# Kernel optimization log

Hardware: AMD Instinct MI355X
Metric: run time of the kernel (lower is better)

Reference implementation:

```python
import jax, jax.numpy as jnp
import numpy as np

N, M, K = 100000, 50000, 8   # num vertices, num hyperedges, fixed hyperedge size
DIN, DOUT = 128, 128

def setup_inputs() -> dict:
    key = jax.random.key(0)
    k1, k2, k3 = jax.random.split(key, 3)
    X = jax.random.normal(k1, (N, DIN), jnp.float32)
    vertex = jax.random.randint(k2, (M * K,), 0, N)          # member vertices, flattened
    edges = jnp.repeat(jnp.arange(M), K)                     # hyperedge id per entry (sorted)
    W = jax.random.normal(k3, (DIN, DOUT), jnp.float32) / np.sqrt(DIN)
    b = jnp.zeros((DOUT,), jnp.float32)
    return {"X": X, "vertex": vertex, "edges": edges, "W": W, "b": b}

def reference(X, vertex, edges, W, b):
    # theta: Linear(in, out) applied BEFORE graph construction (as in dhg.HyperGCNConv)
    Y = X @ W + b                              # [N, DOUT]
    verts = vertex.reshape(M, K)               # hyperedge membership (edges = repeat(arange(M), K))
    feats = Y[verts]                           # [M, K, DOUT] gather
    # pairwise squared distances within each hyperedge
    sq = jnp.sum(feats * feats, axis=-1)                      # [M, K]
    d2 = sq[:, :, None] + sq[:, None, :] - 2.0 * jnp.einsum('mkd,mld->mkl', feats, feats)
    flat = jnp.argmax(d2.reshape(M, K * K), axis=1)
    ui, vi = flat // K, flat % K                              # argmax-distance pair positions
    u = jnp.take_along_axis(verts, ui[:, None], 1)[:, 0]      # [M]
    v = jnp.take_along_axis(verts, vi[:, None], 1)[:, 0]      # [M]
    w = jnp.float32(1.0 / (2 * K - 3))                        # HyperGCN mediator weight
    pos = jnp.arange(K)
    med = ((pos[None, :] != ui[:, None]) & (pos[None, :] != vi[:, None])).astype(Y.dtype)  # [M,K]
    # graph edges: (u,v) + (u,m),(v,m) for each mediator m; masked entries get weight 0
    src = jnp.concatenate([u, jnp.repeat(u, K), jnp.repeat(v, K)])
    dst = jnp.concatenate([v, verts.reshape(-1), verts.reshape(-1)])
    wts = jnp.concatenate([jnp.full((M,), w, Y.dtype), (med * w).reshape(-1), (med * w).reshape(-1)])
    # GCN smoothing: D^{-1/2} (A + I) D^{-1/2} Y with symmetric A, duplicate edges summed
    deg = jnp.ones((N,), Y.dtype).at[src].add(wts).at[dst].add(wts)
    dinv = jax.lax.rsqrt(deg)
    Xs = Y * dinv[:, None]
    out = Xs                                                  # self-loop term
    out = out.at[dst].add(wts[:, None] * Xs[src])
    out = out.at[src].add(wts[:, None] * Xs[dst])
    out = out * dinv[:, None]
    return jax.nn.relu(out)                                   # is_last=False -> ReLU (dropout=0)
```

## Files before the change

kernel.cpp:

```cpp
#include <hip/hip_runtime.h>
#include <hip/hip_bf16.h>

#define NV 100000
#define ME 50000
#define NINC (ME * 8)
#define NBLK ((NV + 255) / 256)
constexpr float WMED = 1.0f / 13.0f;

typedef __attribute__((ext_vector_type(8))) short bf16x8;
typedef __attribute__((ext_vector_type(4))) float f32x4;

static __device__ inline void cvt_split8(const float4& a, const float4& b,
                                         bf16x8& hi, bf16x8& lo) {
    const float v[8] = {a.x, a.y, a.z, a.w, b.x, b.y, b.z, b.w};
    #pragma unroll
    for (int j = 0; j < 8; ++j) {
        __hip_bfloat16 h = __float2bfloat16(v[j]);
        const float hf = __bfloat162float(h);
        __hip_bfloat16 l = __float2bfloat16(v[j] - hf);
        union { __hip_bfloat16 b; short s; } uh{h}, ul{l};
        hi[j] = uh.s;
        lo[j] = ul.s;
    }
}

__global__ __launch_bounds__(256) void k_wsplit(const float* __restrict__ W,
                                                short* __restrict__ Wg) {
    const int idx = blockIdx.x * 256 + threadIdx.x;
    const int k = idx >> 7;
    const int c = idx & 127;
    const float w = W[idx];
    __hip_bfloat16 h = __float2bfloat16(w);
    const float hf = __bfloat162float(h);
    __hip_bfloat16 l = __float2bfloat16(w - hf);
    const int cb = c >> 6, gp = (c >> 4) & 3, m = c & 15;
    const int s = k >> 5, qq = (k >> 3) & 3, j = k & 7;
    const int base = cb * 1024 + (s * 4 + gp) * 64 + qq * 16 + m;
    union { __hip_bfloat16 b; short s; } uh{h}, ul{l};
    Wg[(long)base * 8 + j] = uh.s;
    Wg[(long)(2048 + base) * 8 + j] = ul.s;
}

__global__ __launch_bounds__(512, 4) void k_gemm(const float* __restrict__ X,
                                                 const uint4* __restrict__ Wg,
                                                 const float* __restrict__ bias,
                                                 float* __restrict__ Y,
                                                 __hip_bfloat16* __restrict__ Ybf) {
    __shared__ uint4 sW[2048];
    const int t = threadIdx.x;
    const int wv = t >> 6;
    const int L  = t & 63;
    const int m  = L & 15;
    const int q  = L >> 4;

    const int rb = blockIdx.x >> 1;
    const int cb = blockIdx.x & 1;

    #pragma unroll
    for (int f = 0; f < 4; ++f) {
        const int fi = f * 512 + t;
        const int mat = fi >> 10, loc = fi & 1023;
        sW[fi] = Wg[(long)mat * 2048 + cb * 1024 + loc];
    }

    const int row_base = rb * 256 + wv * 32;
    int r0 = row_base + m;      if (r0 > NV - 1) r0 = NV - 1;
    int r1 = row_base + 16 + m; if (r1 > NV - 1) r1 = NV - 1;
    const float* p0 = X + (long)r0 * 128 + q * 8;
    const float* p1 = X + (long)r1 * 128 + q * 8;

    float4 A[4][4];
    #pragma unroll
    for (int s = 0; s < 4; ++s) {
        A[s][0] = *(const float4*)(p0 + s * 32);
        A[s][1] = *(const float4*)(p0 + s * 32 + 4);
        A[s][2] = *(const float4*)(p1 + s * 32);
        A[s][3] = *(const float4*)(p1 + s * 32 + 4);
    }
    __syncthreads();

    const bf16x8* sWf = (const bf16x8*)sW;

    f32x4 acc[2][4];
    #pragma unroll
    for (int tt = 0; tt < 2; ++tt)
        #pragma unroll
        for (int g = 0; g < 4; ++g)
            acc[tt][g] = (f32x4){0.f, 0.f, 0.f, 0.f};

    #pragma unroll
    for (int s = 0; s < 4; ++s) {
        bf16x8 ah0, al0, ah1, al1;
        cvt_split8(A[s][0], A[s][1], ah0, al0);
        cvt_split8(A[s][2], A[s][3], ah1, al1);
        #pragma unroll
        for (int g = 0; g < 4; ++g) {
            const bf16x8 bh = sWf[(s * 4 + g) * 64 + L];
            const bf16x8 bl = sWf[1024 + (s * 4 + g) * 64 + L];
            acc[0][g] = __builtin_amdgcn_mfma_f32_16x16x32_bf16(ah0, bh, acc[0][g], 0, 0, 0);
            acc[0][g] = __builtin_amdgcn_mfma_f32_16x16x32_bf16(ah0, bl, acc[0][g], 0, 0, 0);
            acc[0][g] = __builtin_amdgcn_mfma_f32_16x16x32_bf16(al0, bh, acc[0][g], 0, 0, 0);
            acc[1][g] = __builtin_amdgcn_mfma_f32_16x16x32_bf16(ah1, bh, acc[1][g], 0, 0, 0);
            acc[1][g] = __builtin_amdgcn_mfma_f32_16x16x32_bf16(ah1, bl, acc[1][g], 0, 0, 0);
            acc[1][g] = __builtin_amdgcn_mfma_f32_16x16x32_bf16(al1, bh, acc[1][g], 0, 0, 0);
        }
    }

    #pragma unroll
    for (int g = 0; g < 4; ++g) {
        const int col = cb * 64 + g * 16 + m;
        const float bc = bias[col];
        #pragma unroll
        for (int tt = 0; tt < 2; ++tt) {
            #pragma unroll
            for (int r = 0; r < 4; ++r) {
                const int row = row_base + tt * 16 + q * 4 + r;
                const float v = acc[tt][g][r] + bc;
                const float vn = __shfl_xor(v, 1);
                if (row < NV) {
                    Y[(long)row * 128 + col] = v;
                    if ((L & 1) == 0) {
                        __hip_bfloat162 h2;
                        h2.x = __float2bfloat16(v);
                        h2.y = __float2bfloat16(vn);
                        *(__hip_bfloat162*)(Ybf + (long)row * 128 + col) = h2;
                    }
                }
            }
        }
    }
}

__global__ __launch_bounds__(256) void k_edge(const float* __restrict__ Y,
                                              const int* __restrict__ vertex,
                                              int* __restrict__ uvpos) {
    __shared__ float sF[4][8 * 132];
    const int wid = threadIdx.x >> 6;
    const int lane = threadIdx.x & 63;
    const int m = blockIdx.x * 4 + wid;
    float* F = sF[wid];

    int verts[8];
    #pragma unroll
    for (int p = 0; p < 8; ++p) verts[p] = vertex[m * 8 + p];

    #pragma unroll
    for (int p = 0; p < 8; ++p) {
        const float2 v = *(const float2*)(Y + (long)verts[p] * 128 + lane * 2);
        *(float2*)(F + p * 132 + lane * 2) = v;
    }
    __syncthreads();

    const int k = lane >> 3, l = lane & 7;

    const int h = (k > l) ? 64 : 0;
    float acc = 0.0f;
    const float4* ra = (const float4*)(F + k * 132 + h);
    const float4* rbp = (const float4*)(F + l * 132 + h);
    #pragma unroll
    for (int d4 = 0; d4 < 16; ++d4) {
        const float4 a = ra[d4], b = rbp[d4];
        acc = fmaf(a.x, b.x, acc);
        acc = fmaf(a.y, b.y, acc);
        acc = fmaf(a.z, b.z, acc);
        acc = fmaf(a.w, b.w, acc);
    }

    float dacc = 0.0f;
    const float4* rd = (const float4*)(F + k * 132 + 64 + l * 8);
    #pragma unroll
    for (int d4 = 0; d4 < 2; ++d4) {
        const float4 a = rd[d4];
        dacc = fmaf(a.x, a.x, dacc);
        dacc = fmaf(a.y, a.y, dacc);
        dacc = fmaf(a.z, a.z, dacc);
        dacc = fmaf(a.w, a.w, dacc);
    }
    dacc += __shfl_xor(dacc, 1);
    dacc += __shfl_xor(dacc, 2);
    dacc += __shfl_xor(dacc, 4);

    const float sqk = __shfl(acc, k * 9) + __shfl(dacc, k * 8);
    const float sql = __shfl(acc, l * 9) + __shfl(dacc, l * 8);
    const float accT = __shfl(acc, l * 8 + k);
    float v = (k == l) ? 0.0f : (sqk + sql - 2.0f * (acc + accT));

    int idx = lane;
    #pragma unroll
    for (int off = 32; off >= 1; off >>= 1) {
        const float ov = __shfl_xor(v, off);
        const int oi = __shfl_xor(idx, off);
        if (ov > v || (ov == v && oi < idx)) { v = ov; idx = oi; }
    }
    if (lane == 0) uvpos[m] = idx;
}

__global__ __launch_bounds__(256) void k_init(int* __restrict__ cnt,
                                              int* __restrict__ rowptr) {
    const int i = blockIdx.x * 256 + threadIdx.x;
    if (i < NV) cnt[i] = 0;
    if (i == 0) rowptr[NV] = NINC;
}

__global__ __launch_bounds__(256) void k_hist(const int* __restrict__ vertex,
                                              int* __restrict__ cnt) {
    const int j = blockIdx.x * 256 + threadIdx.x;
    if (j < NINC) atomicAdd(cnt + vertex[j], 1);
}

__global__ __launch_bounds__(256) void k_scan1(const int* __restrict__ cnt,
                                               int* __restrict__ bsum) {
    __shared__ int s[256];
    const int t = threadIdx.x;
    const int i = blockIdx.x * 256 + t;
    s[t] = (i < NV) ? cnt[i] : 0;
    __syncthreads();
    #pragma unroll
    for (int off = 128; off >= 1; off >>= 1) {
        if (t < off) s[t] += s[t + off];
        __syncthreads();
    }
    if (t == 0) bsum[blockIdx.x] = s[0];
}

__global__ __launch_bounds__(64) void k_scan2(const int* __restrict__ bsum,
                                              int* __restrict__ boff) {
    const int lane = threadIdx.x;
    int running = 0;
    for (int c = 0; c * 64 < NBLK; ++c) {
        const int idx = c * 64 + lane;
        int v = (idx < NBLK) ? bsum[idx] : 0;
        int x = v;
        #pragma unroll
        for (int off = 1; off < 64; off <<= 1) {
            const int n = __shfl_up(x, off);
            if (lane >= off) x += n;
        }
        if (idx < NBLK) boff[idx] = running + x - v;
        running += __shfl(x, 63);
    }
}

__global__ __launch_bounds__(256) void k_scan3(const int* __restrict__ cnt,
                                               const int* __restrict__ boff,
                                               int* __restrict__ rowptr,
                                               int* __restrict__ fill) {
    __shared__ int s[256];
    const int t = threadIdx.x;
    const int i = blockIdx.x * 256 + t;
    const int v = (i < NV) ? cnt[i] : 0;
    s[t] = v;
    __syncthreads();
    #pragma unroll
    for (int off = 1; off < 256; off <<= 1) {
        const int add = (t >= off) ? s[t - off] : 0;
        __syncthreads();
        s[t] += add;
        __syncthreads();
    }
    if (i < NV) {
        const int excl = boff[blockIdx.x] + s[t] - v;
        rowptr[i] = excl;
        fill[i] = excl;
    }
}

__global__ __launch_bounds__(256) void k_fill(const int* __restrict__ vertex,
                                              const int* __restrict__ uvpos,
                                              int* __restrict__ fill,
                                              int* __restrict__ entries) {
    const int j = blockIdx.x * 256 + threadIdx.x;
    if (j < NINC) {
        const int v = vertex[j];
        const int m = j >> 3, p = j & 7;
        const int idx = uvpos[m];
        const int role = (p == (idx >> 3) || p == (idx & 7)) ? 0 : 1;
        const int slot = atomicAdd(fill + v, 1);
        entries[slot] = (m << 1) | role;
    }
}

__global__ __launch_bounds__(256) void k_deg(const int* __restrict__ rowptr,
                                             const int* __restrict__ entries,
                                             float* __restrict__ deg) {
    const int i = blockIdx.x * 256 + threadIdx.x;
    if (i >= NV) return;
    const int start = rowptr[i], end = rowptr[i + 1];
    float d = 1.0f;
    for (int e = start; e < end; ++e)
        d += (entries[e] & 1) ? (2.0f * WMED) : (7.0f * WMED);
    deg[i] = d;
}

__global__ __launch_bounds__(256) void k_sp(const __hip_bfloat16* __restrict__ Ybf,
                                            const int* __restrict__ vertex,
                                            const int* __restrict__ uvpos,
                                            const float* __restrict__ deg,
                                            __hip_bfloat162* __restrict__ SP) {
    const int wid = threadIdx.x >> 6;
    const int lane = threadIdx.x & 63;
    const int m = blockIdx.x * 4 + wid;

    const int idx = uvpos[m];
    const int ui = idx >> 3, vi = idx & 7;

    float S0 = 0.f, S1 = 0.f, U0 = 0.f, U1 = 0.f, V0 = 0.f, V1 = 0.f;
    #pragma unroll
    for (int p = 0; p < 8; ++p) {
        const int vp = vertex[m * 8 + p];
        const float di = rsqrtf(deg[vp]);
        const __hip_bfloat162 y2 =
            ((const __hip_bfloat162*)(Ybf + (long)vp * 128))[lane];
        const float r0 = __bfloat162float(y2.x) * di;
        const float r1 = __bfloat162float(y2.y) * di;
        S0 += r0; S1 += r1;
        if (p == ui) { U0 = r0; U1 = r1; }
        if (p == vi) { V0 = r0; V1 = r1; }
    }
    __hip_bfloat162 s2, p2;
    s2.x = __float2bfloat16(WMED * S0);
    s2.y = __float2bfloat16(WMED * S1);
    p2.x = __float2bfloat16(WMED * (U0 + V0));
    p2.y = __float2bfloat16(WMED * (U1 + V1));
    SP[(long)(2 * m) * 64 + lane] = s2;
    SP[(long)(2 * m + 1) * 64 + lane] = p2;
}

__global__ __launch_bounds__(256) void k_gather(const float* __restrict__ Y,
                                                const float* __restrict__ deg,
                                                const int* __restrict__ rowptr,
                                                const int* __restrict__ entries,
                                                const __hip_bfloat162* __restrict__ SP,
                                                float* __restrict__ out) {
    const int wid = threadIdx.x >> 6;
    const int lane = threadIdx.x & 63;
    const int i = blockIdx.x * 4 + wid;

    const int start = rowptr[i], end = rowptr[i + 1];
    const int degc = end - start;
    const int tl = (lane < degc) ? entries[start + lane] : 0;

    const float din = rsqrtf(deg[i]);
    const float2 y = *(const float2*)(Y + (long)i * 128 + lane * 2);
    const float xs0 = y.x * din;
    const float xs1 = y.y * din;

    float a0 = 0.f, a1 = 0.f;
    float fnuv = 0.f;
    const int dmain = (degc < 64) ? degc : 64;

    for (int e = 0; e < dmain; e += 4) {
        const int j1 = (e + 1 < dmain) ? e + 1 : e;
        const int j2 = (e + 2 < dmain) ? e + 2 : e;
        const int j3 = (e + 3 < dmain) ? e + 3 : e;
        const float m1 = (e + 1 < dmain) ? 1.f : 0.f;
        const float m2 = (e + 2 < dmain) ? 1.f : 0.f;
        const float m3 = (e + 3 < dmain) ? 1.f : 0.f;
        const int t0 = __shfl(tl, e);
        const int t1 = __shfl(tl, j1);
        const int t2 = __shfl(tl, j2);
        const int t3 = __shfl(tl, j3);
        const __hip_bfloat162 T0 = SP[(long)t0 * 64 + lane];
        const __hip_bfloat162 T1 = SP[(long)t1 * 64 + lane];
        const __hip_bfloat162 T2 = SP[(long)t2 * 64 + lane];
        const __hip_bfloat162 T3 = SP[(long)t3 * 64 + lane];
        fnuv += (float)((t0 & 1) ^ 1) + m1 * (float)((t1 & 1) ^ 1)
              + m2 * (float)((t2 & 1) ^ 1) + m3 * (float)((t3 & 1) ^ 1);
        a0 += __bfloat162float(T0.x) + m1 * __bfloat162float(T1.x)
            + m2 * __bfloat162float(T2.x) + m3 * __bfloat162float(T3.x);
        a1 += __bfloat162float(T0.y) + m1 * __bfloat162float(T1.y)
            + m2 * __bfloat162float(T2.y) + m3 * __bfloat162float(T3.y);
    }
    for (int e2 = start + 64; e2 < end; ++e2) {
        const int t = entries[e2];
        const __hip_bfloat162 T = SP[(long)t * 64 + lane];
        fnuv += (float)((t & 1) ^ 1);
        a0 += __bfloat162float(T.x);
        a1 += __bfloat162float(T.y);
    }

    const float self = 1.0f - WMED * fnuv;
    a0 = fmaf(self, xs0, a0);
    a1 = fmaf(self, xs1, a1);
    float2 o;
    o.x = fmaxf(a0 * din, 0.0f);
    o.y = fmaxf(a1 * din, 0.0f);
    *(float2*)(out + (long)i * 128 + lane * 2) = o;
}

extern "C" void kernel_launch(void* const* d_in, const int* in_sizes, int n_in,
                              void* d_out, int out_size, void* d_ws, size_t ws_size,
                              hipStream_t stream) {
    const float* X      = (const float*)d_in[0];
    const int*   vertex = (const int*)d_in[1];
    const float* W      = (const float*)d_in[3];
    const float* bias   = (const float*)d_in[4];
    float* out = (float*)d_out;

    float* Y              = (float*)d_ws;
    __hip_bfloat16* Ybf   = (__hip_bfloat16*)(Y + (long)NV * 128);
    __hip_bfloat162* SP   = (__hip_bfloat162*)(Ybf + (long)NV * 128);
    float* deg            = (float*)((__hip_bfloat16*)SP + (long)2 * ME * 128);
    int*   uvpos          = (int*)(deg + NV);
    int*   cnt            = uvpos + ME;
    int*   rowptr         = cnt + NV;
    int*   fill           = rowptr + NV + 1;
    int*   bsum           = fill + NV;
    int*   boff           = bsum + NBLK;
    int*   entries        = boff + NBLK;
    char*  pW             = (char*)(entries + NINC);
    uint4* Wg             = (uint4*)(((uintptr_t)pW + 15) & ~(uintptr_t)15);

    k_wsplit<<<64, 256, 0, stream>>>(W, (short*)Wg);
    k_gemm <<<NBLK * 2, 512, 0, stream>>>(X, Wg, bias, Y, Ybf);
    k_edge <<<ME / 4, 256, 0, stream>>>(Y, vertex, uvpos);
    k_init <<<NBLK, 256, 0, stream>>>(cnt, rowptr);
    k_hist <<<(NINC + 255) / 256, 256, 0, stream>>>(vertex, cnt);
    k_scan1<<<NBLK, 256, 0, stream>>>(cnt, bsum);
    k_scan2<<<1, 64, 0, stream>>>(bsum, boff);
    k_scan3<<<NBLK, 256, 0, stream>>>(cnt, boff, rowptr, fill);
    k_fill <<<(NINC + 255) / 256, 256, 0, stream>>>(vertex, uvpos, fill, entries);
    k_deg  <<<NBLK, 256, 0, stream>>>(rowptr, entries, deg);
    k_sp   <<<ME / 4, 256, 0, stream>>>(Ybf, vertex, uvpos, deg, SP);
    k_gather<<<NV / 4, 256, 0, stream>>>(Y, deg, rowptr, entries, SP, out);
}
```

Baseline: 274.5 us.

## Read GEMM weights from global, prefetch X per k-step, vectorize edge-kernel loads

The GEMM no longer stages the split bf16 weights in shared memory. Each lane reads its weight fragments straight from global memory, which should be served by cache. Blocks shrink to 256 threads over 128 rows, and the X tile for the next k-step is prefetched while the current one is converted and multiplied. The edge kernel gathers member features as float4 across half-waves, computes the upper-half squared norms during the load, and drops the block barrier, relying on each wave touching only its own shared-memory region. The risks are more global weight traffic per block and reliance on ordering of shared-memory accesses within a wave.

```diff
diff --git a/kernel.cpp b/kernel.cpp
--- a/kernel.cpp
+++ b/kernel.cpp
@@ -5,6 +5,7 @@
 #define ME 50000
 #define NINC (ME * 8)
 #define NBLK ((NV + 255) / 256)
+#define NRBG ((NV + 127) / 128)
 constexpr float WMED = 1.0f / 13.0f;
 
 typedef __attribute__((ext_vector_type(8))) short bf16x8;
@@ -41,12 +42,11 @@
     Wg[(long)(2048 + base) * 8 + j] = ul.s;
 }
 
-__global__ __launch_bounds__(512, 4) void k_gemm(const float* __restrict__ X,
+__global__ __launch_bounds__(256, 4) void k_gemm(const float* __restrict__ X,
                                                  const uint4* __restrict__ Wg,
                                                  const float* __restrict__ bias,
                                                  float* __restrict__ Y,
                                                  __hip_bfloat16* __restrict__ Ybf) {
-    __shared__ uint4 sW[2048];
     const int t = threadIdx.x;
     const int wv = t >> 6;
     const int L  = t & 63;
@@ -56,30 +56,14 @@
     const int rb = blockIdx.x >> 1;
     const int cb = blockIdx.x & 1;
 
-    #pragma unroll
-    for (int f = 0; f < 4; ++f) {
-        const int fi = f * 512 + t;
-        const int mat = fi >> 10, loc = fi & 1023;
-        sW[fi] = Wg[(long)mat * 2048 + cb * 1024 + loc];
-    }
-
-    const int row_base = rb * 256 + wv * 32;
+    const int row_base = rb * 128 + wv * 32;
     int r0 = row_base + m;      if (r0 > NV - 1) r0 = NV - 1;
     int r1 = row_base + 16 + m; if (r1 > NV - 1) r1 = NV - 1;
     const float* p0 = X + (long)r0 * 128 + q * 8;
     const float* p1 = X + (long)r1 * 128 + q * 8;
 
-    float4 A[4][4];
-    #pragma unroll
-    for (int s = 0; s < 4; ++s) {
-        A[s][0] = *(const float4*)(p0 + s * 32);
-        A[s][1] = *(const float4*)(p0 + s * 32 + 4);
-        A[s][2] = *(const float4*)(p1 + s * 32);
-        A[s][3] = *(const float4*)(p1 + s * 32 + 4);
-    }
-    __syncthreads();
-
-    const bf16x8* sWf = (const bf16x8*)sW;
+    const bf16x8* Whf = (const bf16x8*)Wg + cb * 1024;
+    const bf16x8* Wlf = (const bf16x8*)Wg + 2048 + cb * 1024;
 
     f32x4 acc[2][4];
     #pragma unroll
@@ -88,15 +72,27 @@
         for (int g = 0; g < 4; ++g)
             acc[tt][g] = (f32x4){0.f, 0.f, 0.f, 0.f};
 
+    float4 Ac0 = *(const float4*)(p0);
+    float4 Ac1 = *(const float4*)(p0 + 4);
+    float4 Ac2 = *(const float4*)(p1);
+    float4 Ac3 = *(const float4*)(p1 + 4);
+
     #pragma unroll
     for (int s = 0; s < 4; ++s) {
+        float4 An0, An1, An2, An3;
+        if (s < 3) {
+            An0 = *(const float4*)(p0 + (s + 1) * 32);
+            An1 = *(const float4*)(p0 + (s + 1) * 32 + 4);
+            An2 = *(const float4*)(p1 + (s + 1) * 32);
+            An3 = *(const float4*)(p1 + (s + 1) * 32 + 4);
+        }
         bf16x8 ah0, al0, ah1, al1;
-        cvt_split8(A[s][0], A[s][1], ah0, al0);
-        cvt_split8(A[s][2], A[s][3], ah1, al1);
+        cvt_split8(Ac0, Ac1, ah0, al0);
+        cvt_split8(Ac2, Ac3, ah1, al1);
         #pragma unroll
         for (int g = 0; g < 4; ++g) {
-            const bf16x8 bh = sWf[(s * 4 + g) * 64 + L];
-            const bf16x8 bl = sWf[1024 + (s * 4 + g) * 64 + L];
+            const bf16x8 bh = Whf[(s * 4 + g) * 64 + L];
+            const bf16x8 bl = Wlf[(s * 4 + g) * 64 + L];
             acc[0][g] = __builtin_amdgcn_mfma_f32_16x16x32_bf16(ah0, bh, acc[0][g], 0, 0, 0);
             acc[0][g] = __builtin_amdgcn_mfma_f32_16x16x32_bf16(ah0, bl, acc[0][g], 0, 0, 0);
             acc[0][g] = __builtin_amdgcn_mfma_f32_16x16x32_bf16(al0, bh, acc[0][g], 0, 0, 0);
@@ -104,26 +100,35 @@
             acc[1][g] = __builtin_amdgcn_mfma_f32_16x16x32_bf16(ah1, bl, acc[1][g], 0, 0, 0);
             acc[1][g] = __builtin_amdgcn_mfma_f32_16x16x32_bf16(al1, bh, acc[1][g], 0, 0, 0);
         }
-    }
-
-    #pragma unroll
-    for (int g = 0; g < 4; ++g) {
-        const int col = cb * 64 + g * 16 + m;
-        const float bc = bias[col];
-        #pragma unroll
-        for (int tt = 0; tt < 2; ++tt) {
+        if (s < 3) { Ac0 = An0; Ac1 = An1; Ac2 = An2; Ac3 = An3; }
+    }
+
+    float bc[4];
+    #pragma unroll
+    for (int g = 0; g < 4; ++g) bc[g] = bias[cb * 64 + g * 16 + m];
+
+    #pragma unroll
+    for (int tt = 0; tt < 2; ++tt) {
+        #pragma unroll
+        for (int r = 0; r < 4; ++r) {
+            const int row = row_base + tt * 16 + q * 4 + r;
+            float vg[4], vn[4];
             #pragma unroll
-            for (int r = 0; r < 4; ++r) {
-                const int row = row_base + tt * 16 + q * 4 + r;
-                const float v = acc[tt][g][r] + bc;
-                const float vn = __shfl_xor(v, 1);
-                if (row < NV) {
-                    Y[(long)row * 128 + col] = v;
-                    if ((L & 1) == 0) {
+            for (int g = 0; g < 4; ++g) {
+                vg[g] = acc[tt][g][r] + bc[g];
+                vn[g] = __shfl_xor(vg[g], 1);
+            }
+            if (row < NV) {
+                #pragma unroll
+                for (int g = 0; g < 4; ++g)
+                    Y[(long)row * 128 + cb * 64 + g * 16 + m] = vg[g];
+                if ((L & 1) == 0) {
+                    #pragma unroll
+                    for (int g = 0; g < 4; ++g) {
                         __hip_bfloat162 h2;
-                        h2.x = __float2bfloat16(v);
-                        h2.y = __float2bfloat16(vn);
-                        *(__hip_bfloat162*)(Ybf + (long)row * 128 + col) = h2;
+                        h2.x = __float2bfloat16(vg[g]);
+                        h2.y = __float2bfloat16(vn[g]);
+                        *(__hip_bfloat162*)(Ybf + (long)row * 128 + cb * 64 + g * 16 + m) = h2;
                     }
                 }
             }
@@ -134,22 +139,35 @@
 __global__ __launch_bounds__(256) void k_edge(const float* __restrict__ Y,
                                               const int* __restrict__ vertex,
                                               int* __restrict__ uvpos) {
-    __shared__ float sF[4][8 * 132];
+    __shared__ float sF[4][8 * 132 + 8];
     const int wid = threadIdx.x >> 6;
     const int lane = threadIdx.x & 63;
     const int m = blockIdx.x * 4 + wid;
     float* F = sF[wid];
-
-    int verts[8];
-    #pragma unroll
-    for (int p = 0; p < 8; ++p) verts[p] = vertex[m * 8 + p];
-
-    #pragma unroll
-    for (int p = 0; p < 8; ++p) {
-        const float2 v = *(const float2*)(Y + (long)verts[p] * 128 + lane * 2);
-        *(float2*)(F + p * 132 + lane * 2) = v;
-    }
-    __syncthreads();
+    float* T8 = F + 8 * 132;
+
+    const int c = lane & 31;
+    const int half = lane >> 5;
+
+    float part[4];
+    #pragma unroll
+    for (int i = 0; i < 4; ++i) {
+        const int row = 2 * i + half;
+        const int vr = vertex[m * 8 + row];
+        const float4 v = *(const float4*)(Y + (long)vr * 128 + c * 4);
+        *(float4*)(F + row * 132 + c * 4) = v;
+        const float s = v.x * v.x + v.y * v.y + v.z * v.z + v.w * v.w;
+        part[i] = (c >= 16) ? s : 0.0f;
+    }
+    #pragma unroll
+    for (int off = 1; off <= 8; off <<= 1) {
+        #pragma unroll
+        for (int i = 0; i < 4; ++i) part[i] += __shfl_xor(part[i], off);
+    }
+    if (c == 16) {
+        #pragma unroll
+        for (int i = 0; i < 4; ++i) T8[2 * i + half] = part[i];
+    }
 
     const int k = lane >> 3, l = lane & 7;
 
@@ -166,24 +184,13 @@
         acc = fmaf(a.w, b.w, acc);
     }
 
-    float dacc = 0.0f;
-    const float4* rd = (const float4*)(F + k * 132 + 64 + l * 8);
-    #pragma unroll
-    for (int d4 = 0; d4 < 2; ++d4) {
-        const float4 a = rd[d4];
-        dacc = fmaf(a.x, a.x, dacc);
-        dacc = fmaf(a.y, a.y, dacc);
-        dacc = fmaf(a.z, a.z, dacc);
-        dacc = fmaf(a.w, a.w, dacc);
-    }
-    dacc += __shfl_xor(dacc, 1);
-    dacc += __shfl_xor(dacc, 2);
-    dacc += __shfl_xor(dacc, 4);
-
-    const float sqk = __shfl(acc, k * 9) + __shfl(dacc, k * 8);
-    const float sql = __shfl(acc, l * 9) + __shfl(dacc, l * 8);
     const float accT = __shfl(acc, l * 8 + k);
-    float v = (k == l) ? 0.0f : (sqk + sql - 2.0f * (acc + accT));
+    const float s1k = __shfl(acc, k * 9);
+    const float s1l = __shfl(acc, l * 9);
+    const float Tk = T8[k];
+    const float Tl = T8[l];
+    float v = (k == l) ? 0.0f
+                       : ((s1k + Tk) + (s1l + Tl) - 2.0f * (acc + accT));
 
     int idx = lane;
     #pragma unroll
@@ -412,7 +419,7 @@
     uint4* Wg             = (uint4*)(((uintptr_t)pW + 15) & ~(uintptr_t)15);
 
     k_wsplit<<<64, 256, 0, stream>>>(W, (short*)Wg);
-    k_gemm <<<NBLK * 2, 512, 0, stream>>>(X, Wg, bias, Y, Ybf);
+    k_gemm <<<NRBG * 2, 256, 0, stream>>>(X, Wg, bias, Y, Ybf);
     k_edge <<<ME / 4, 256, 0, stream>>>(Y, vertex, uvpos);
     k_init <<<NBLK, 256, 0, stream>>>(cnt, rowptr);
     k_hist <<<(NINC + 255) / 256, 256, 0, stream>>>(vertex, cnt);
```

After: 276.8 us. About the same (+0.8%).
